# Optimization experiments

Hardware: AMD Instinct MI355X
Metric: run time of the kernel (lower is better)

The kernel has to match this reference:

```python
import jax, jax.numpy as jnp
import numpy as np

B, S, D, H = 1, 2048, 1024, 16
DK = D // H  # 64


def setup_inputs() -> dict:
    key = jax.random.key(0)
    ks = jax.random.split(key, 11)
    s = 1.0 / np.sqrt(D)
    return {
        "q": jax.random.normal(ks[0], (B, S, D), jnp.float32),
        "k": jax.random.normal(ks[1], (B, S, D), jnp.float32),
        "v": jax.random.normal(ks[2], (B, S, D), jnp.float32),
        "mask": jnp.ones((B, 1, 1, S), jnp.int32),
        "Wq": jax.random.normal(ks[3], (D, D), jnp.float32) * s,
        "bq": jnp.zeros((D,), jnp.float32),
        "Wk": jax.random.normal(ks[4], (D, D), jnp.float32) * s,
        "bk": jnp.zeros((D,), jnp.float32),
        "Wv": jax.random.normal(ks[5], (D, D), jnp.float32) * s,
        "bv": jnp.zeros((D,), jnp.float32),
        "Wo": jax.random.normal(ks[6], (D, D), jnp.float32) * s,
        "bo": jnp.zeros((D,), jnp.float32),
    }


def reference(q, k, v, mask, Wq, bq, Wk, bk, Wv, bv, Wo, bo):
    # torch Linear convention: y = x @ W.T + b
    def split_heads(x, W, b):
        y = x @ W.T + b                     # (B,S,D)
        return y.reshape(B, -1, H, DK).transpose(0, 2, 1, 3)  # (B,H,S,DK)

    qh = split_heads(q, Wq, bq)
    kh = split_heads(k, Wk, bk)
    vh = split_heads(v, Wv, bv)
    scores = jnp.einsum('bhqd,bhkd->bhqk', qh, kh) / jnp.sqrt(jnp.float32(DK))
    scores = jnp.where(mask == 0, jnp.float32(-1e9), scores)
    attn_weights = jax.nn.softmax(scores, axis=-1)   # (B,H,Sq,Sk)
    ctx = jnp.einsum('bhqk,bhkd->bhqd', attn_weights, vh)
    ctx = ctx.transpose(0, 2, 1, 3).reshape(B, -1, D)
    out = ctx @ Wo.T + bo                            # dropout = identity (eval)
    return out, attn_weights
```

## Files before the change

kernel.cpp:

```cpp
#include <hip/hip_runtime.h>
#include <hip/hip_bf16.h>

#define S 2048
#define D 1024
#define H 16
#define DK 64

typedef __bf16 bf16x8 __attribute__((ext_vector_type(8)));
typedef __bf16 bf16x4 __attribute__((ext_vector_type(4)));
typedef float f32x4 __attribute__((ext_vector_type(4)));

#define LDT 72
#define LDTP 136

#define MFMA(a, b, c) __builtin_amdgcn_mfma_f32_16x16x32_bf16((a), (b), (c), 0, 0, 0)

__device__ __forceinline__ void attn_decode(int L, int& h, int& q0) {
  const int xcd = L & 7, slot = L >> 3;
  h = xcd + 8 * (slot >> 5);
  q0 = (slot & 31) * 64;
}

__global__ __launch_bounds__(256) void conv_bf16(
    const float* __restrict__ q, const float* __restrict__ k,
    const float* __restrict__ v, const float* __restrict__ wq,
    const float* __restrict__ wk, const float* __restrict__ wv,
    const float* __restrict__ wo, __bf16* __restrict__ qb,
    __bf16* __restrict__ kb, __bf16* __restrict__ vb,
    __bf16* __restrict__ wqb, __bf16* __restrict__ wkb,
    __bf16* __restrict__ wvb, __bf16* __restrict__ wob) {
  const size_t SD = (size_t)S * D, DD = (size_t)D * D;
  size_t i = ((size_t)blockIdx.x * 256 + threadIdx.x) * 8;
  const float* src;
  __bf16* dst;
  size_t off;
  if (i < SD) {
    src = q; dst = qb; off = i;
  } else if (i < 2 * SD) {
    src = k; dst = kb; off = i - SD;
  } else if (i < 3 * SD) {
    src = v; dst = vb; off = i - 2 * SD;
  } else if (i < 3 * SD + DD) {
    src = wq; dst = wqb; off = i - 3 * SD;
  } else if (i < 3 * SD + 2 * DD) {
    src = wk; dst = wkb; off = i - 3 * SD - DD;
  } else if (i < 3 * SD + 3 * DD) {
    src = wv; dst = wvb; off = i - 3 * SD - 2 * DD;
  } else {
    src = wo; dst = wob; off = i - 3 * SD - 3 * DD;
  }
  float4 f0 = *(const float4*)(src + off);
  float4 f1 = *(const float4*)(src + off + 4);
  bf16x8 o;
  o[0] = (__bf16)f0.x; o[1] = (__bf16)f0.y; o[2] = (__bf16)f0.z; o[3] = (__bf16)f0.w;
  o[4] = (__bf16)f1.x; o[5] = (__bf16)f1.y; o[6] = (__bf16)f1.z; o[7] = (__bf16)f1.w;
  *(bf16x8*)(dst + off) = o;
}

__global__ __launch_bounds__(256) void proj_qkv(
    const __bf16* __restrict__ qb, const __bf16* __restrict__ kb,
    const __bf16* __restrict__ vb, const __bf16* __restrict__ Wqb,
    const __bf16* __restrict__ Wkb, const __bf16* __restrict__ Wvb,
    const float* __restrict__ bq, const float* __restrict__ bk,
    const float* __restrict__ bv, __bf16* __restrict__ Qh,
    __bf16* __restrict__ Kh, __bf16* __restrict__ Vt) {
  __shared__ __bf16 Xs[64 * LDT];
  __shared__ __bf16 Ws[64 * LDT];
  const int z = blockIdx.z;
  const __bf16* X = (z == 0) ? qb : (z == 1) ? kb : vb;
  const __bf16* W = (z == 0) ? Wqb : (z == 1) ? Wkb : Wvb;
  const float* bias = (z == 0) ? bq : (z == 1) ? bk : bv;

  const int t = threadIdx.x;
  const int lane = t & 63, wid = t >> 6;
  const int m0 = blockIdx.y * 64, n0 = blockIdx.x * 64;
  const int srow = t >> 2, scol = (t & 3) * 16;
  const int wm = (wid >> 1) * 32, wn = (wid & 1) * 32;
  const int fm = lane & 15, fk = (lane >> 4) * 8, r0 = (lane >> 4) * 4;

  f32x4 acc[2][2] = {};

  for (int k0 = 0; k0 < D; k0 += 64) {
    const __bf16* xs = X + (size_t)(m0 + srow) * D + k0 + scol;
    *(bf16x8*)&Xs[srow * LDT + scol] = *(const bf16x8*)xs;
    *(bf16x8*)&Xs[srow * LDT + scol + 8] = *(const bf16x8*)(xs + 8);
    const __bf16* ws = W + (size_t)(n0 + srow) * D + k0 + scol;
    *(bf16x8*)&Ws[srow * LDT + scol] = *(const bf16x8*)ws;
    *(bf16x8*)&Ws[srow * LDT + scol + 8] = *(const bf16x8*)(ws + 8);
    __syncthreads();
#pragma unroll
    for (int ks = 0; ks < 2; ++ks) {
      const int kb2 = ks * 32 + fk;
      bf16x8 a0 = *(const bf16x8*)&Xs[(wm + fm) * LDT + kb2];
      bf16x8 a1 = *(const bf16x8*)&Xs[(wm + 16 + fm) * LDT + kb2];
      bf16x8 b0 = *(const bf16x8*)&Ws[(wn + fm) * LDT + kb2];
      bf16x8 b1 = *(const bf16x8*)&Ws[(wn + 16 + fm) * LDT + kb2];
      acc[0][0] = MFMA(a0, b0, acc[0][0]);
      acc[0][1] = MFMA(a0, b1, acc[0][1]);
      acc[1][0] = MFMA(a1, b0, acc[1][0]);
      acc[1][1] = MFMA(a1, b1, acc[1][1]);
    }
    __syncthreads();
  }

#pragma unroll
  for (int mi = 0; mi < 2; ++mi) {
#pragma unroll
    for (int ni = 0; ni < 2; ++ni) {
      const int n = n0 + wn + ni * 16 + fm;
      const float bn = bias[n];
      if (z == 2) {
        const int mrow = m0 + wm + mi * 16 + r0;
        bf16x4 pk;
#pragma unroll
        for (int r = 0; r < 4; ++r) pk[r] = (__bf16)(acc[mi][ni][r] + bn);
        *(bf16x4*)&Vt[(size_t)(n >> 6) * DK * S + (size_t)(n & 63) * S + mrow] = pk;
      } else {
        __bf16* Y = (z == 0) ? Qh : Kh;
#pragma unroll
        for (int r = 0; r < 4; ++r) {
          const int m = m0 + wm + mi * 16 + r0 + r;
          Y[(size_t)(n >> 6) * S * DK + (size_t)m * DK + (n & 63)] =
              (__bf16)(acc[mi][ni][r] + bn);
        }
      }
    }
  }
}

__global__ __launch_bounds__(256) void proj_out(
    const __bf16* __restrict__ X, const __bf16* __restrict__ W,
    const float* __restrict__ bias, float* __restrict__ Y) {
  __shared__ __bf16 Xs[64 * LDT];
  __shared__ __bf16 Ws[64 * LDT];
  const int t = threadIdx.x;
  const int lane = t & 63, wid = t >> 6;
  const int m0 = blockIdx.y * 64, n0 = blockIdx.x * 64;
  const int srow = t >> 2, scol = (t & 3) * 16;
  const int wm = (wid >> 1) * 32, wn = (wid & 1) * 32;
  const int fm = lane & 15, fk = (lane >> 4) * 8, r0 = (lane >> 4) * 4;

  f32x4 acc[2][2] = {};

  for (int k0 = 0; k0 < D; k0 += 64) {
    const __bf16* xs = X + (size_t)(m0 + srow) * D + k0 + scol;
    *(bf16x8*)&Xs[srow * LDT + scol] = *(const bf16x8*)xs;
    *(bf16x8*)&Xs[srow * LDT + scol + 8] = *(const bf16x8*)(xs + 8);
    const __bf16* ws = W + (size_t)(n0 + srow) * D + k0 + scol;
    *(bf16x8*)&Ws[srow * LDT + scol] = *(const bf16x8*)ws;
    *(bf16x8*)&Ws[srow * LDT + scol + 8] = *(const bf16x8*)(ws + 8);
    __syncthreads();
#pragma unroll
    for (int ks = 0; ks < 2; ++ks) {
      const int kb2 = ks * 32 + fk;
      bf16x8 a0 = *(const bf16x8*)&Xs[(wm + fm) * LDT + kb2];
      bf16x8 a1 = *(const bf16x8*)&Xs[(wm + 16 + fm) * LDT + kb2];
      bf16x8 b0 = *(const bf16x8*)&Ws[(wn + fm) * LDT + kb2];
      bf16x8 b1 = *(const bf16x8*)&Ws[(wn + 16 + fm) * LDT + kb2];
      acc[0][0] = MFMA(a0, b0, acc[0][0]);
      acc[0][1] = MFMA(a0, b1, acc[0][1]);
      acc[1][0] = MFMA(a1, b0, acc[1][0]);
      acc[1][1] = MFMA(a1, b1, acc[1][1]);
    }
    __syncthreads();
  }

#pragma unroll
  for (int mi = 0; mi < 2; ++mi) {
#pragma unroll
    for (int ni = 0; ni < 2; ++ni) {
      const int n = n0 + wn + ni * 16 + fm;
      const float bn = bias[n];
#pragma unroll
      for (int r = 0; r < 4; ++r) {
        const int m = m0 + wm + mi * 16 + r0 + r;
        Y[(size_t)m * D + n] = acc[mi][ni][r] + bn;
      }
    }
  }
}

__global__ __launch_bounds__(512, 4) void attn_sum(
    const __bf16* __restrict__ Qh, const __bf16* __restrict__ Kh,
    const int* __restrict__ mask, float* __restrict__ linv) {
  __shared__ __bf16 Qs[64 * LDT];
  __shared__ __bf16 Ks[128 * LDT];
  __shared__ float lred[2][64];
  const int t = threadIdx.x, lane = t & 63, wid = t >> 6;
  const int qg = wid & 3, kh = wid >> 2;
  int h, q0;
  attn_decode(blockIdx.x, h, q0);
  const int fm = lane & 15, fk = (lane >> 4) * 8, r0 = (lane >> 4) * 4;
  const __bf16* Qg = Qh + (size_t)h * S * DK;
  const __bf16* Kg = Kh + (size_t)h * S * DK;
  {
    const int qr = t >> 3, qc = (t & 7) * 8;
    *(bf16x8*)&Qs[qr * LDT + qc] = *(const bf16x8*)(Qg + (size_t)(q0 + qr) * DK + qc);
  }
  const int srow = t >> 2, scol = (t & 3) * 16;
  float lacc[4] = {0.f, 0.f, 0.f, 0.f};

  for (int k0 = 0; k0 < S; k0 += 128) {
    __syncthreads();
    {
      const __bf16* src = Kg + (size_t)(k0 + srow) * DK + scol;
      *(bf16x8*)&Ks[srow * LDT + scol] = *(const bf16x8*)src;
      *(bf16x8*)&Ks[srow * LDT + scol + 8] = *(const bf16x8*)(src + 8);
    }
    __syncthreads();
    f32x4 acc[4] = {};
    __builtin_amdgcn_s_setprio(1);
#pragma unroll
    for (int ks = 0; ks < 2; ++ks) {
      const int kb = ks * 32 + fk;
      bf16x8 a = *(const bf16x8*)&Qs[(qg * 16 + fm) * LDT + kb];
#pragma unroll
      for (int nt = 0; nt < 4; ++nt) {
        bf16x8 b = *(const bf16x8*)&Ks[(kh * 64 + nt * 16 + fm) * LDT + kb];
        acc[nt] = MFMA(a, b, acc[nt]);
      }
    }
    __builtin_amdgcn_s_setprio(0);
#pragma unroll
    for (int nt = 0; nt < 4; ++nt) {
      const int mk = mask[k0 + kh * 64 + nt * 16 + fm];
#pragma unroll
      for (int r = 0; r < 4; ++r)
        lacc[r] += __expf(mk ? acc[nt][r] * 0.125f : -1e9f);
    }
  }
#pragma unroll
  for (int r = 0; r < 4; ++r) {
    float ps = lacc[r];
    ps += __shfl_xor(ps, 1, 64);
    ps += __shfl_xor(ps, 2, 64);
    ps += __shfl_xor(ps, 4, 64);
    ps += __shfl_xor(ps, 8, 64);
    lacc[r] = ps;
  }
  if (fm == 0) {
#pragma unroll
    for (int r = 0; r < 4; ++r) lred[kh][qg * 16 + r0 + r] = lacc[r];
  }
  __syncthreads();
  if (t < 64) linv[(size_t)h * S + q0 + t] = 1.0f / (lred[0][t] + lred[1][t]);
}

__global__ __launch_bounds__(512, 4) void attn_ctx(
    const __bf16* __restrict__ Qh, const __bf16* __restrict__ Kh,
    const __bf16* __restrict__ Vt, const int* __restrict__ mask,
    const float* __restrict__ linv, float* __restrict__ attn,
    __bf16* __restrict__ ctx) {
  __shared__ __align__(16) char smem[62464];
  __bf16* Qs = (__bf16*)smem;
  __bf16* Ks = (__bf16*)(smem + 9216);
  __bf16* Vs = (__bf16*)(smem + 27648);
  __bf16* Ps = (__bf16*)(smem + 45056);
  const int t = threadIdx.x, lane = t & 63, wid = t >> 6;
  const int qg = wid & 3, kh = wid >> 2;
  int h, q0;
  attn_decode(blockIdx.x, h, q0);
  const int fm = lane & 15, fk = (lane >> 4) * 8, r0 = (lane >> 4) * 4;
  const __bf16* Qg = Qh + (size_t)h * S * DK;
  const __bf16* Kg = Kh + (size_t)h * S * DK;
  const __bf16* Vg = Vt + (size_t)h * DK * S;
  float* attnH = attn + (size_t)h * S * S;

  {
    const int qr = t >> 3, qc = (t & 7) * 8;
    *(bf16x8*)&Qs[qr * LDT + qc] = *(const bf16x8*)(Qg + (size_t)(q0 + qr) * DK + qc);
  }
  float invl[4];
#pragma unroll
  for (int r = 0; r < 4; ++r)
    invl[r] = linv[(size_t)h * S + q0 + qg * 16 + r0 + r];

  const int srow = t >> 2, scol = (t & 3) * 16;
  const int vrow = t >> 3, vcol = (t & 7) * 16;
  const int arow = t >> 3, ac0 = (t & 7) * 4;
  f32x4 cacc[4] = {};

  for (int k0 = 0; k0 < S; k0 += 128) {
    __syncthreads();
    {
      const __bf16* src = Kg + (size_t)(k0 + srow) * DK + scol;
      *(bf16x8*)&Ks[srow * LDT + scol] = *(const bf16x8*)src;
      *(bf16x8*)&Ks[srow * LDT + scol + 8] = *(const bf16x8*)(src + 8);
      const __bf16* vsrc = Vg + (size_t)vrow * S + k0 + vcol;
      *(bf16x8*)&Vs[vrow * LDTP + vcol] = *(const bf16x8*)vsrc;
      *(bf16x8*)&Vs[vrow * LDTP + vcol + 8] = *(const bf16x8*)(vsrc + 8);
    }
    __syncthreads();
    f32x4 acc[4] = {};
    __builtin_amdgcn_s_setprio(1);
#pragma unroll
    for (int ks = 0; ks < 2; ++ks) {
      const int kb = ks * 32 + fk;
      bf16x8 a = *(const bf16x8*)&Qs[(qg * 16 + fm) * LDT + kb];
#pragma unroll
      for (int nt = 0; nt < 4; ++nt) {
        bf16x8 b = *(const bf16x8*)&Ks[(kh * 64 + nt * 16 + fm) * LDT + kb];
        acc[nt] = MFMA(a, b, acc[nt]);
      }
    }
    __builtin_amdgcn_s_setprio(0);
#pragma unroll
    for (int nt = 0; nt < 4; ++nt) {
      const int kc = kh * 64 + nt * 16 + fm;
      const int mk = mask[k0 + kc];
#pragma unroll
      for (int r = 0; r < 4; ++r) {
        const float sv = mk ? acc[nt][r] * 0.125f : -1e9f;
        const float p = __expf(sv) * invl[r];
        Ps[(qg * 16 + r0 + r) * LDTP + kc] = (__bf16)p;
      }
    }
    __syncthreads();
    __builtin_amdgcn_s_setprio(1);
#pragma unroll
    for (int ks = 0; ks < 2; ++ks) {
      const int kb = kh * 64 + ks * 32 + fk;
      bf16x8 a = *(const bf16x8*)&Ps[(qg * 16 + fm) * LDTP + kb];
#pragma unroll
      for (int nt = 0; nt < 4; ++nt) {
        bf16x8 b = *(const bf16x8*)&Vs[(nt * 16 + fm) * LDTP + kb];
        cacc[nt] = MFMA(a, b, cacc[nt]);
      }
    }
    __builtin_amdgcn_s_setprio(0);
    {
      float* dst = attnH + (size_t)(q0 + arow) * S + k0;
      const __bf16* srcP = &Ps[arow * LDTP];
#pragma unroll
      for (int i = 0; i < 4; ++i) {
        bf16x4 pv4 = *(const bf16x4*)&srcP[ac0 + i * 32];
        f32x4 o;
        o[0] = (float)pv4[0]; o[1] = (float)pv4[1];
        o[2] = (float)pv4[2]; o[3] = (float)pv4[3];
        __builtin_nontemporal_store(o, (f32x4*)&dst[ac0 + i * 32]);
      }
    }
  }

  __syncthreads();
  float* sc = (float*)smem;
  if (kh == 1) {
#pragma unroll
    for (int nt = 0; nt < 4; ++nt)
#pragma unroll
      for (int r = 0; r < 4; ++r)
        sc[(qg * 16 + r0 + r) * 68 + nt * 16 + fm] = cacc[nt][r];
  }
  __syncthreads();
  if (kh == 0) {
#pragma unroll
    for (int nt = 0; nt < 4; ++nt)
#pragma unroll
      for (int r = 0; r < 4; ++r) {
        const int qrow = qg * 16 + r0 + r;
        const float val = cacc[nt][r] + sc[qrow * 68 + nt * 16 + fm];
        ctx[(size_t)(q0 + qrow) * D + h * DK + nt * 16 + fm] = (__bf16)val;
      }
  }
}

extern "C" void kernel_launch(void* const* d_in, const int* in_sizes, int n_in,
                              void* d_out, int out_size, void* d_ws,
                              size_t ws_size, hipStream_t stream) {
  const float* q = (const float*)d_in[0];
  const float* k = (const float*)d_in[1];
  const float* v = (const float*)d_in[2];
  const int* mask = (const int*)d_in[3];
  const float* Wq = (const float*)d_in[4];
  const float* bq = (const float*)d_in[5];
  const float* Wk = (const float*)d_in[6];
  const float* bk = (const float*)d_in[7];
  const float* Wv = (const float*)d_in[8];
  const float* bv = (const float*)d_in[9];
  const float* Wo = (const float*)d_in[10];
  const float* bo = (const float*)d_in[11];

  float* out = (float*)d_out;
  float* attn = out + (size_t)S * D;

  __bf16* qb = (__bf16*)d_ws;
  __bf16* kb = qb + (size_t)S * D;
  __bf16* vb = kb + (size_t)S * D;
  __bf16* Wqb = vb + (size_t)S * D;
  __bf16* Wkb = Wqb + (size_t)D * D;
  __bf16* Wvb = Wkb + (size_t)D * D;
  __bf16* Wob = Wvb + (size_t)D * D;
  __bf16* Qh = Wob + (size_t)D * D;
  __bf16* Kh = Qh + (size_t)S * D;
  __bf16* Vt = Kh + (size_t)S * D;
  __bf16* ctxb = Vt + (size_t)S * D;
  float* linv = (float*)(ctxb + (size_t)S * D);

  const int conv_blocks = (3 * S * D + 4 * D * D) / (8 * 256);
  conv_bf16<<<conv_blocks, 256, 0, stream>>>(q, k, v, Wq, Wk, Wv, Wo, qb, kb,
                                             vb, Wqb, Wkb, Wvb, Wob);

  dim3 pgrid(D / 64, S / 64, 3);
  proj_qkv<<<pgrid, 256, 0, stream>>>(qb, kb, vb, Wqb, Wkb, Wvb, bq, bk, bv,
                                      Qh, Kh, Vt);

  attn_sum<<<S / 64 * H, 512, 0, stream>>>(Qh, Kh, mask, linv);
  attn_ctx<<<S / 64 * H, 512, 0, stream>>>(Qh, Kh, Vt, mask, linv, attn, ctxb);

  dim3 ogrid(D / 64, S / 64);
  proj_out<<<ogrid, 256, 0, stream>>>(ctxb, Wob, bo, out);
}
```

Baseline: 398.7 us.

## Use 128x128 GEMM tiles and store attention probs directly from transposed MFMA

The QKV and output projection GEMMs move from 64x64 to 128x128 block tiles, with each wave computing a 64x64 sub-tile (4x4 MFMAs), for more operand reuse per LDS load. In attn_ctx the QK^T MFMA operands are swapped, so each lane holds four consecutive key columns of one query row. That lets the fp32 attention weights be written straight from registers with vectorized nontemporal stores and the mask be read as int4. This drops the separate LDS readback pass that converted bf16 P back to fp32, and the stored weights now keep full fp32 precision instead of bf16-rounded values. The trade-off is fewer projection blocks (e.g. 384 for QKV, 128 for the output) and higher register pressure, which may hurt occupancy and load balance.

```diff
diff --git a/kernel.cpp b/kernel.cpp
--- a/kernel.cpp
+++ b/kernel.cpp
@@ -64,8 +64,8 @@
     const float* __restrict__ bq, const float* __restrict__ bk,
     const float* __restrict__ bv, __bf16* __restrict__ Qh,
     __bf16* __restrict__ Kh, __bf16* __restrict__ Vt) {
-  __shared__ __bf16 Xs[64 * LDT];
-  __shared__ __bf16 Ws[64 * LDT];
+  __shared__ __bf16 Xs[128 * LDT];
+  __shared__ __bf16 Ws[128 * LDT];
   const int z = blockIdx.z;
   const __bf16* X = (z == 0) ? qb : (z == 1) ? kb : vb;
   const __bf16* W = (z == 0) ? Wqb : (z == 1) ? Wkb : Wvb;
@@ -73,40 +73,44 @@
 
   const int t = threadIdx.x;
   const int lane = t & 63, wid = t >> 6;
-  const int m0 = blockIdx.y * 64, n0 = blockIdx.x * 64;
-  const int srow = t >> 2, scol = (t & 3) * 16;
-  const int wm = (wid >> 1) * 32, wn = (wid & 1) * 32;
+  const int m0 = blockIdx.y * 128, n0 = blockIdx.x * 128;
+  const int srow = t >> 1, scol = (t & 1) * 32;
+  const int wm = (wid >> 1) * 64, wn = (wid & 1) * 64;
   const int fm = lane & 15, fk = (lane >> 4) * 8, r0 = (lane >> 4) * 4;
 
-  f32x4 acc[2][2] = {};
+  f32x4 acc[4][4] = {};
 
   for (int k0 = 0; k0 < D; k0 += 64) {
     const __bf16* xs = X + (size_t)(m0 + srow) * D + k0 + scol;
-    *(bf16x8*)&Xs[srow * LDT + scol] = *(const bf16x8*)xs;
-    *(bf16x8*)&Xs[srow * LDT + scol + 8] = *(const bf16x8*)(xs + 8);
     const __bf16* ws = W + (size_t)(n0 + srow) * D + k0 + scol;
-    *(bf16x8*)&Ws[srow * LDT + scol] = *(const bf16x8*)ws;
-    *(bf16x8*)&Ws[srow * LDT + scol + 8] = *(const bf16x8*)(ws + 8);
+#pragma unroll
+    for (int i = 0; i < 4; ++i) {
+      *(bf16x8*)&Xs[srow * LDT + scol + i * 8] = *(const bf16x8*)(xs + i * 8);
+      *(bf16x8*)&Ws[srow * LDT + scol + i * 8] = *(const bf16x8*)(ws + i * 8);
+    }
     __syncthreads();
 #pragma unroll
     for (int ks = 0; ks < 2; ++ks) {
       const int kb2 = ks * 32 + fk;
-      bf16x8 a0 = *(const bf16x8*)&Xs[(wm + fm) * LDT + kb2];
-      bf16x8 a1 = *(const bf16x8*)&Xs[(wm + 16 + fm) * LDT + kb2];
-      bf16x8 b0 = *(const bf16x8*)&Ws[(wn + fm) * LDT + kb2];
-      bf16x8 b1 = *(const bf16x8*)&Ws[(wn + 16 + fm) * LDT + kb2];
-      acc[0][0] = MFMA(a0, b0, acc[0][0]);
-      acc[0][1] = MFMA(a0, b1, acc[0][1]);
-      acc[1][0] = MFMA(a1, b0, acc[1][0]);
-      acc[1][1] = MFMA(a1, b1, acc[1][1]);
-    }
-    __syncthreads();
-  }
-
-#pragma unroll
-  for (int mi = 0; mi < 2; ++mi) {
-#pragma unroll
-    for (int ni = 0; ni < 2; ++ni) {
+      bf16x8 a[4], b[4];
+#pragma unroll
+      for (int i = 0; i < 4; ++i) {
+        a[i] = *(const bf16x8*)&Xs[(wm + i * 16 + fm) * LDT + kb2];
+        b[i] = *(const bf16x8*)&Ws[(wn + i * 16 + fm) * LDT + kb2];
+      }
+#pragma unroll
+      for (int mi = 0; mi < 4; ++mi)
+#pragma unroll
+        for (int ni = 0; ni < 4; ++ni)
+          acc[mi][ni] = MFMA(a[mi], b[ni], acc[mi][ni]);
+    }
+    __syncthreads();
+  }
+
+#pragma unroll
+  for (int mi = 0; mi < 4; ++mi) {
+#pragma unroll
+    for (int ni = 0; ni < 4; ++ni) {
       const int n = n0 + wn + ni * 16 + fm;
       const float bn = bias[n];
       if (z == 2) {
@@ -131,44 +135,48 @@
 __global__ __launch_bounds__(256) void proj_out(
     const __bf16* __restrict__ X, const __bf16* __restrict__ W,
     const float* __restrict__ bias, float* __restrict__ Y) {
-  __shared__ __bf16 Xs[64 * LDT];
-  __shared__ __bf16 Ws[64 * LDT];
+  __shared__ __bf16 Xs[128 * LDT];
+  __shared__ __bf16 Ws[128 * LDT];
   const int t = threadIdx.x;
   const int lane = t & 63, wid = t >> 6;
-  const int m0 = blockIdx.y * 64, n0 = blockIdx.x * 64;
-  const int srow = t >> 2, scol = (t & 3) * 16;
-  const int wm = (wid >> 1) * 32, wn = (wid & 1) * 32;
+  const int m0 = blockIdx.y * 128, n0 = blockIdx.x * 128;
+  const int srow = t >> 1, scol = (t & 1) * 32;
+  const int wm = (wid >> 1) * 64, wn = (wid & 1) * 64;
   const int fm = lane & 15, fk = (lane >> 4) * 8, r0 = (lane >> 4) * 4;
 
-  f32x4 acc[2][2] = {};
+  f32x4 acc[4][4] = {};
 
   for (int k0 = 0; k0 < D; k0 += 64) {
     const __bf16* xs = X + (size_t)(m0 + srow) * D + k0 + scol;
-    *(bf16x8*)&Xs[srow * LDT + scol] = *(const bf16x8*)xs;
-    *(bf16x8*)&Xs[srow * LDT + scol + 8] = *(const bf16x8*)(xs + 8);
     const __bf16* ws = W + (size_t)(n0 + srow) * D + k0 + scol;
-    *(bf16x8*)&Ws[srow * LDT + scol] = *(const bf16x8*)ws;
-    *(bf16x8*)&Ws[srow * LDT + scol + 8] = *(const bf16x8*)(ws + 8);
+#pragma unroll
+    for (int i = 0; i < 4; ++i) {
+      *(bf16x8*)&Xs[srow * LDT + scol + i * 8] = *(const bf16x8*)(xs + i * 8);
+      *(bf16x8*)&Ws[srow * LDT + scol + i * 8] = *(const bf16x8*)(ws + i * 8);
+    }
     __syncthreads();
 #pragma unroll
     for (int ks = 0; ks < 2; ++ks) {
       const int kb2 = ks * 32 + fk;
-      bf16x8 a0 = *(const bf16x8*)&Xs[(wm + fm) * LDT + kb2];
-      bf16x8 a1 = *(const bf16x8*)&Xs[(wm + 16 + fm) * LDT + kb2];
-      bf16x8 b0 = *(const bf16x8*)&Ws[(wn + fm) * LDT + kb2];
-      bf16x8 b1 = *(const bf16x8*)&Ws[(wn + 16 + fm) * LDT + kb2];
-      acc[0][0] = MFMA(a0, b0, acc[0][0]);
-      acc[0][1] = MFMA(a0, b1, acc[0][1]);
-      acc[1][0] = MFMA(a1, b0, acc[1][0]);
-      acc[1][1] = MFMA(a1, b1, acc[1][1]);
-    }
-    __syncthreads();
-  }
-
-#pragma unroll
-  for (int mi = 0; mi < 2; ++mi) {
-#pragma unroll
-    for (int ni = 0; ni < 2; ++ni) {
+      bf16x8 a[4], b[4];
+#pragma unroll
+      for (int i = 0; i < 4; ++i) {
+        a[i] = *(const bf16x8*)&Xs[(wm + i * 16 + fm) * LDT + kb2];
+        b[i] = *(const bf16x8*)&Ws[(wn + i * 16 + fm) * LDT + kb2];
+      }
+#pragma unroll
+      for (int mi = 0; mi < 4; ++mi)
+#pragma unroll
+        for (int ni = 0; ni < 4; ++ni)
+          acc[mi][ni] = MFMA(a[mi], b[ni], acc[mi][ni]);
+    }
+    __syncthreads();
+  }
+
+#pragma unroll
+  for (int mi = 0; mi < 4; ++mi) {
+#pragma unroll
+    for (int ni = 0; ni < 4; ++ni) {
       const int n = n0 + wn + ni * 16 + fm;
       const float bn = bias[n];
 #pragma unroll
@@ -270,14 +278,11 @@
     const int qr = t >> 3, qc = (t & 7) * 8;
     *(bf16x8*)&Qs[qr * LDT + qc] = *(const bf16x8*)(Qg + (size_t)(q0 + qr) * DK + qc);
   }
-  float invl[4];
-#pragma unroll
-  for (int r = 0; r < 4; ++r)
-    invl[r] = linv[(size_t)h * S + q0 + qg * 16 + r0 + r];
+  const int qcol = qg * 16 + fm;
+  const float invl_s = linv[(size_t)h * S + q0 + qcol];
 
   const int srow = t >> 2, scol = (t & 3) * 16;
   const int vrow = t >> 3, vcol = (t & 7) * 16;
-  const int arow = t >> 3, ac0 = (t & 7) * 4;
   f32x4 cacc[4] = {};
 
   for (int k0 = 0; k0 < S; k0 += 128) {
@@ -296,24 +301,31 @@
 #pragma unroll
     for (int ks = 0; ks < 2; ++ks) {
       const int kb = ks * 32 + fk;
-      bf16x8 a = *(const bf16x8*)&Qs[(qg * 16 + fm) * LDT + kb];
+      bf16x8 qf = *(const bf16x8*)&Qs[qcol * LDT + kb];
 #pragma unroll
       for (int nt = 0; nt < 4; ++nt) {
-        bf16x8 b = *(const bf16x8*)&Ks[(kh * 64 + nt * 16 + fm) * LDT + kb];
-        acc[nt] = MFMA(a, b, acc[nt]);
+        bf16x8 kf = *(const bf16x8*)&Ks[(kh * 64 + nt * 16 + fm) * LDT + kb];
+        acc[nt] = MFMA(kf, qf, acc[nt]);
       }
     }
     __builtin_amdgcn_s_setprio(0);
 #pragma unroll
     for (int nt = 0; nt < 4; ++nt) {
-      const int kc = kh * 64 + nt * 16 + fm;
-      const int mk = mask[k0 + kc];
+      const int kc = kh * 64 + nt * 16 + r0;
+      const int4 mk4 = *(const int4*)&mask[k0 + kc];
+      const int mka[4] = {mk4.x, mk4.y, mk4.z, mk4.w};
+      f32x4 p4;
+      bf16x4 pb;
 #pragma unroll
       for (int r = 0; r < 4; ++r) {
-        const float sv = mk ? acc[nt][r] * 0.125f : -1e9f;
-        const float p = __expf(sv) * invl[r];
-        Ps[(qg * 16 + r0 + r) * LDTP + kc] = (__bf16)p;
-      }
+        const float sv = mka[r] ? acc[nt][r] * 0.125f : -1e9f;
+        const float p = __expf(sv) * invl_s;
+        p4[r] = p;
+        pb[r] = (__bf16)p;
+      }
+      __builtin_nontemporal_store(
+          p4, (f32x4*)&attnH[(size_t)(q0 + qcol) * S + k0 + kc]);
+      *(bf16x4*)&Ps[qcol * LDTP + kc] = pb;
     }
     __syncthreads();
     __builtin_amdgcn_s_setprio(1);
@@ -328,18 +340,6 @@
       }
     }
     __builtin_amdgcn_s_setprio(0);
-    {
-      float* dst = attnH + (size_t)(q0 + arow) * S + k0;
-      const __bf16* srcP = &Ps[arow * LDTP];
-#pragma unroll
-      for (int i = 0; i < 4; ++i) {
-        bf16x4 pv4 = *(const bf16x4*)&srcP[ac0 + i * 32];
-        f32x4 o;
-        o[0] = (float)pv4[0]; o[1] = (float)pv4[1];
-        o[2] = (float)pv4[2]; o[3] = (float)pv4[3];
-        __builtin_nontemporal_store(o, (f32x4*)&dst[ac0 + i * 32]);
-      }
-    }
   }
 
   __syncthreads();
@@ -400,13 +400,13 @@
   conv_bf16<<<conv_blocks, 256, 0, stream>>>(q, k, v, Wq, Wk, Wv, Wo, qb, kb,
                                              vb, Wqb, Wkb, Wvb, Wob);
 
-  dim3 pgrid(D / 64, S / 64, 3);
+  dim3 pgrid(D / 128, S / 128, 3);
   proj_qkv<<<pgrid, 256, 0, stream>>>(qb, kb, vb, Wqb, Wkb, Wvb, bq, bk, bv,
                                       Qh, Kh, Vt);
 
   attn_sum<<<S / 64 * H, 512, 0, stream>>>(Qh, Kh, mask, linv);
   attn_ctx<<<S / 64 * H, 512, 0, stream>>>(Qh, Kh, Vt, mask, linv, attn, ctxb);
 
-  dim3 ogrid(D / 64, S / 64);
+  dim3 ogrid(D / 128, S / 128);
   proj_out<<<ogrid, 256, 0, stream>>>(ctxb, Wob, bo, out);
 }
```

Result: slower. 429.7 us (+7.8%).
